# Optimization experiments

Measured on AMD Instinct MI355X. Metric: run time of the kernel, lower is better.

## Reference

```python
import jax, jax.numpy as jnp
import numpy as np

N, C, H, W = 8, 256, 52, 52
N_WIN, NUM_HEADS, TOPK = 7, 1, 4
RS = (H // N_WIN, W // N_WIN)  # region size (7, 7)
SCALE = C ** -0.5


def _avg_pool_ceil(t):
    # F.avg_pool2d(kernel=RS, stride=RS, ceil_mode=True, count_include_pad=False)
    B, Ch, h_in, w_in = t.shape
    h = -(-h_in // RS[0]); w = -(-w_in // RS[1])
    tp = jnp.pad(t, ((0, 0), (0, 0), (0, h * RS[0] - h_in), (0, w * RS[1] - w_in)))
    s = tp.reshape(B, Ch, h, RS[0], w, RS[1]).sum(axis=(3, 5))
    rc = np.minimum(RS[0], h_in - np.arange(h) * RS[0]).astype(np.float32)
    cc = np.minimum(RS[1], w_in - np.arange(w) * RS[1]).astype(np.float32)
    return s / (rc[:, None] * cc[None, :])


def _nearest_up(t):
    # F.interpolate(mode='nearest', scale_factor=RS) for integer scales == repeat
    return jnp.repeat(jnp.repeat(t, RS[0], axis=2), RS[1], axis=3)


def _grid2seq(t):
    # BCHW -> (B, nhead, nregion, reg_area, head_dim)
    B, Ch, Hp, Wp = t.shape
    rh, rw = Hp // RS[0], Wp // RS[1]
    hd = Ch // NUM_HEADS
    t = t.reshape(B, NUM_HEADS, hd, rh, RS[0], rw, RS[1]).transpose(0, 1, 3, 5, 4, 6, 2)
    return t.reshape(B, NUM_HEADS, rh * rw, RS[0] * RS[1], hd), rh, rw


def _forward(x, y, q_w, q_b, k_w, k_b):
    q = jnp.einsum('nchw,oc->nohw', x, q_w) + q_b[None, :, None, None]
    k = jnp.einsum('nchw,oc->nohw', y, k_w) + k_b[None, :, None, None]
    # routing path uses detached q, k
    q_r = _avg_pool_ceil(jax.lax.stop_gradient(q))  # (B, C, 8, 8)
    k_r = _avg_pool_ceil(jax.lax.stop_gradient(k))
    B, _, h, w = q_r.shape
    nreg = h * w
    a_r = jnp.einsum('nchw,ncyx->nhwyx', q_r, k_r).reshape(B, nreg, nreg)
    idx = jax.lax.top_k(a_r, TOPK)[1]                              # (B, nreg, topk)
    idx = jnp.broadcast_to(idx[:, None], (B, NUM_HEADS, nreg, TOPK))
    a_r = SCALE * a_r
    # coarse scores upsampled over key pixels, then over query pixels
    a1 = _nearest_up(a_r.reshape(B, nreg, h, w))                   # (B, nreg, Hp, Wp)
    Hp, Wp = a1.shape[2], a1.shape[3]
    a1 = _nearest_up(a1.transpose(0, 2, 3, 1).reshape(B, Hp * Wp, h, w))  # (B, Hp*Wp, Hp, Wp)
    reg_area = (Hp * Wp) // nreg
    a6 = a1.reshape(B, NUM_HEADS, nreg, reg_area // NUM_HEADS, nreg, reg_area)
    # fine attention on padded q, k
    pad_b = (RS[0] - H % RS[0]) % RS[0]
    pad_r = (RS[1] - W % RS[1]) % RS[1]
    qp = jnp.pad(q, ((0, 0), (0, 0), (0, pad_b), (0, pad_r)))
    kp = jnp.pad(k, ((0, 0), (0, 0), (0, pad_b), (0, pad_r)))
    q_seq, rh, rw = _grid2seq(qp)   # (B, nh, nreg, reg_area, hd)
    k_seq, _, _ = _grid2seq(kp)
    bI = jnp.arange(B)[:, None, None, None]
    mI = jnp.arange(NUM_HEADS)[None, :, None, None]
    key_g = k_seq[bI, mI, idx]      # gather top-k key regions: (B, nh, nreg, topk, reg_area, hd)
    attn = jnp.einsum('bmrqd,bmrtkd->bmrqtk', q_seq * SCALE, key_g)
    # torch.scatter along dim 4 with index repeated over the t' axis -> duplicate
    # writes to the same slot; serial torch scatter keeps the LAST write (t'=TOPK-1)
    vals = attn[:, :, :, :TOPK, TOPK - 1, :]  # (B, nh, nreg, topk, reg_area)
    rI = jnp.arange(nreg)[None, None, :, None]
    tI = jnp.arange(TOPK)[None, None, None, :]
    corr = a6.at[bI, mI, rI, tI, idx].set(vals)
    # _corr2grid: 10-dim view + 'bmhwpqyxcd->bmhpwqycxd'
    c10 = corr.reshape(B, NUM_HEADS, rh, rw, RS[0], RS[1], rh, rw, RS[0], RS[1])
    c10 = c10.transpose(0, 1, 2, 4, 3, 5, 6, 8, 7, 9)
    Hf, Wf = rh * RS[0], rw * RS[1]
    corr = c10.reshape(B, NUM_HEADS, Hf, Wf, Hf, Wf)
    corr = corr[:, :, :Hf - pad_b, :Wf - pad_r, :Hf - pad_b, :Wf - pad_r]
    return corr.transpose(0, 2, 3, 1, 4, 5)  # (B, H, W, nhead, H, W)


def setup_inputs():
    ks = jax.random.split(jax.random.key(0), 6)
    return {
        'x': jax.random.normal(ks[0], (N, C, H, W), jnp.float32),
        'y': jax.random.normal(ks[1], (N, C, H, W), jnp.float32),
        'q_w': jax.random.normal(ks[2], (C, C), jnp.float32) * (C ** -0.5),
        'q_b': jax.random.normal(ks[3], (C,), jnp.float32) * 0.02,
        'k_w': jax.random.normal(ks[4], (C, C), jnp.float32) * (C ** -0.5),
        'k_b': jax.random.normal(ks[5], (C,), jnp.float32) * 0.02,
    }


def reference(x, y, q_w, q_b, k_w, k_b):
    return _forward(x, y, q_w, q_b, k_w, k_b)
```

## Files before the change

kernel.cpp:

```cpp
#include <hip/hip_runtime.h>

#define NB 8
#define C 256
#define HW 52
#define P (HW*HW)
#define NREG 64
#define NTOPK 4
#define SCALE 0.0625f

static __device__ __forceinline__ int d7(int v)  { return (v*9363) >> 16; }
static __device__ __forceinline__ int d56(int v) { return (v*18725) >> 20; }
static __device__ __forceinline__ int d13(int v) { return (v*10083) >> 17; }

__global__ __launch_bounds__(256) void k1_pool_prep_tr(
    const float* __restrict__ x, const float* __restrict__ y,
    const float* __restrict__ qw, const float* __restrict__ qb,
    const float* __restrict__ kw, const float* __restrict__ kb,
    float* __restrict__ xr, float* __restrict__ yr, float* __restrict__ xg,
    float* __restrict__ M, float* __restrict__ u, float* __restrict__ v2,
    float* __restrict__ c0p, float* __restrict__ yT)
{
    __shared__ float sm[4*P];
    const int tid = threadIdx.x;
    const int bx = blockIdx.x;

    if (bx >= 1089) {
        const int tb = bx - 1089;
        const int b = tb / 172;
        const int rem = tb - b*172;
        const int ct = rem / 43;
        const int pt = rem - ct*43;
        const int c0 = ct*64, pos0 = pt*64;
        float* tile = sm;
        const float* ysrc = y + ((size_t)(b*256 + c0))*P;
        #pragma unroll
        for (int p = 0; p < 4; p++) {
            const int cr = p*16 + (tid>>4);
            const int f4 = tid&15;
            const int pos = pos0 + f4*4;
            if (pos < P) {
                const float4 v = *(const float4*)(ysrc + (size_t)cr*P + pos);
                float* d = tile + cr*65 + f4*4;
                d[0]=v.x; d[1]=v.y; d[2]=v.z; d[3]=v.w;
            }
        }
        __syncthreads();
        #pragma unroll
        for (int p = 0; p < 4; p++) {
            const int pj = p*16 + (tid>>4);
            const int c4 = tid&15;
            const int pos = pos0 + pj;
            if (pos < P) {
                float4 v;
                v.x = tile[(c4*4+0)*65 + pj];
                v.y = tile[(c4*4+1)*65 + pj];
                v.z = tile[(c4*4+2)*65 + pj];
                v.w = tile[(c4*4+3)*65 + pj];
                *(float4*)(yT + ((size_t)(b*P + pos))*256 + c0 + c4*4) = v;
            }
        }
        return;
    }

    if (bx >= 1024) {
        const int pb = bx - 1024;
        if (pb == 64) {
            float ua = 0.f, va = 0.f;
            for (int e = 0; e < 256; e++) {
                ua += qb[e] * kw[e*256 + tid];
                va += kb[e] * qw[e*256 + tid];
            }
            u[tid] = ua; v2[tid] = va;
            if (tid == 0) {
                float c = 0.f;
                for (int e = 0; e < 256; e++) c += qb[e]*kb[e];
                c0p[0] = c;
            }
            return;
        }
        const int cx0 = pb * 4;
        float (*wqs)[4] = (float(*)[4])sm;
        *(float4*)&wqs[tid][0] = *(const float4*)(qw + tid*256 + cx0);
        __syncthreads();
        float a0=0.f, a1=0.f, a2=0.f, a3=0.f;
        #pragma unroll 4
        for (int o = 0; o < 256; o++) {
            const float wk = kw[o*256 + tid];
            const float4 wq = *(const float4*)&wqs[o][0];
            a0 += wq.x*wk; a1 += wq.y*wk; a2 += wq.z*wk; a3 += wq.w*wk;
        }
        M[(cx0+0)*256 + tid] = a0;
        M[(cx0+1)*256 + tid] = a1;
        M[(cx0+2)*256 + tid] = a2;
        M[(cx0+3)*256 + tid] = a3;
        return;
    }

    const int w = tid >> 6, lane = tid & 63;
    const int pl = bx*4 + w;
    const int proj = pl >> 11;
    const int bcid = pl & 2047;
    const float* src = (proj ? y : x) + (size_t)bcid * P;
    float* plane = sm + w*P;
    {
        const float4* s4 = (const float4*)src;
        float4* p4 = (float4*)plane;
        for (int g = lane; g < 676; g += 64) p4[g] = s4[g];
    }
    __syncthreads();
    const int jh = lane >> 3, jw = lane & 7;
    const int y0 = jh*7, x0 = jw*7;
    const int ry = min(7, HW - y0), rx = min(7, HW - x0);
    float s = 0.f;
    for (int dy = 0; dy < ry; ++dy) {
        const float* row = plane + (y0 + dy)*HW + x0;
        for (int dx = 0; dx < rx; ++dx) s += row[dx];
    }
    (proj ? yr : xr)[bcid*64 + lane] = s / (float)(ry*rx);
    if (!proj) {
        const float* r0 = plane + y0*HW + x0;
        float4 g4;
        g4.x = r0[0]; g4.y = r0[1]; g4.z = r0[2];
        g4.w = (x0 + 3 < HW) ? r0[3] : 0.f;
        *(float4*)&xg[bcid*256 + lane*4] = g4;
    }
}

__global__ __launch_bounds__(256) void k2_gemms(
    const float* __restrict__ xr, const float* __restrict__ yr,
    const float* __restrict__ qw, const float* __restrict__ qb,
    const float* __restrict__ kw, const float* __restrict__ kb,
    float* __restrict__ qr, float* __restrict__ kr,
    const float* __restrict__ xg, const float* __restrict__ M,
    const float* __restrict__ u, float* __restrict__ G)
{
    __shared__ float As[32][64];
    __shared__ float Bs[32][64];
    const int tid = threadIdx.x;
    const int tx = tid & 15, ty = tid >> 4;

    float acc[4][4];
    #pragma unroll
    for (int i = 0; i < 4; i++)
        #pragma unroll
        for (int j = 0; j < 4; j++) acc[i][j] = 0.f;

    if (blockIdx.x < 64) {
        const int bp = blockIdx.x >> 2;
        const int b = bp >> 1, proj = bp & 1;
        const float* X = (proj ? yr : xr) + b*C*64;
        const float* W = proj ? kw : qw;
        const float* Bv = proj ? kb : qb;
        float* O = (proj ? kr : qr) + b*C*64;
        const int o0 = (blockIdx.x & 3) * 64;

        const int aor = tid & 63;
        const int akc = (tid >> 6) * 8;
        const int bkr = tid >> 3;
        const int bjc = (tid & 7) * 8;

        for (int k0 = 0; k0 < 256; k0 += 32) {
            const float4 w0 = *(const float4*)(W + (o0 + aor)*256 + k0 + akc);
            const float4 w1 = *(const float4*)(W + (o0 + aor)*256 + k0 + akc + 4);
            const float4 x0v = *(const float4*)(X + (k0 + bkr)*64 + bjc);
            const float4 x1v = *(const float4*)(X + (k0 + bkr)*64 + bjc + 4);
            __syncthreads();
            As[akc+0][aor] = w0.x; As[akc+1][aor] = w0.y; As[akc+2][aor] = w0.z; As[akc+3][aor] = w0.w;
            As[akc+4][aor] = w1.x; As[akc+5][aor] = w1.y; As[akc+6][aor] = w1.z; As[akc+7][aor] = w1.w;
            *(float4*)&Bs[bkr][bjc] = x0v;
            *(float4*)&Bs[bkr][bjc+4] = x1v;
            __syncthreads();
            #pragma unroll
            for (int kk = 0; kk < 32; kk++) {
                const float4 a = *(const float4*)&As[kk][ty*4];
                const float4 bb = *(const float4*)&Bs[kk][tx*4];
                const float av[4] = {a.x, a.y, a.z, a.w};
                const float bv[4] = {bb.x, bb.y, bb.z, bb.w};
                #pragma unroll
                for (int i = 0; i < 4; i++)
                    #pragma unroll
                    for (int j = 0; j < 4; j++) acc[i][j] += av[i]*bv[j];
            }
        }
        #pragma unroll
        for (int i = 0; i < 4; i++) {
            const int o = o0 + ty*4 + i;
            const float bias = Bv[o];
            float4 ov;
            ov.x = acc[i][0]+bias; ov.y = acc[i][1]+bias;
            ov.z = acc[i][2]+bias; ov.w = acc[i][3]+bias;
            *(float4*)(O + o*64 + tx*4) = ov;
        }
    } else {
        const int id2 = blockIdx.x - 64;
        const int b = id2 >> 4, sub = id2 & 15;
        const int p0 = (sub >> 2)*64, o0 = (sub & 3)*64;
        const float* Xg = xg + b*C*256;
        float* Gb = G + b*256*256;

        const int lkr = tid >> 3;
        const int ljc = (tid & 7) * 8;

        for (int k0 = 0; k0 < 256; k0 += 32) {
            const float4 a0 = *(const float4*)(Xg + (k0 + lkr)*256 + p0 + ljc);
            const float4 a1 = *(const float4*)(Xg + (k0 + lkr)*256 + p0 + ljc + 4);
            const float4 b0 = *(const float4*)(M + (k0 + lkr)*256 + o0 + ljc);
            const float4 b1 = *(const float4*)(M + (k0 + lkr)*256 + o0 + ljc + 4);
            __syncthreads();
            *(float4*)&As[lkr][ljc] = a0; *(float4*)&As[lkr][ljc+4] = a1;
            *(float4*)&Bs[lkr][ljc] = b0; *(float4*)&Bs[lkr][ljc+4] = b1;
            __syncthreads();
            #pragma unroll
            for (int kk = 0; kk < 32; kk++) {
                const float4 a = *(const float4*)&As[kk][ty*4];
                const float4 bb = *(const float4*)&Bs[kk][tx*4];
                const float av[4] = {a.x, a.y, a.z, a.w};
                const float bv[4] = {bb.x, bb.y, bb.z, bb.w};
                #pragma unroll
                for (int i = 0; i < 4; i++)
                    #pragma unroll
                    for (int j = 0; j < 4; j++) acc[i][j] += av[i]*bv[j];
            }
        }
        const float4 u4 = *(const float4*)(u + o0 + tx*4);
        #pragma unroll
        for (int i = 0; i < 4; i++) {
            float4 ov;
            ov.x = acc[i][0]+u4.x; ov.y = acc[i][1]+u4.y;
            ov.z = acc[i][2]+u4.z; ov.w = acc[i][3]+u4.w;
            *(float4*)(Gb + (p0 + ty*4 + i)*256 + o0 + tx*4) = ov;
        }
    }
}

__global__ __launch_bounds__(256) void k3_topk_vals(
    const float* __restrict__ yT, const float* __restrict__ qr,
    const float* __restrict__ kr, const float* __restrict__ G,
    const float* __restrict__ xg, const float* __restrict__ v2,
    const float* __restrict__ c0p,
    float* __restrict__ arT, int* __restrict__ idxout, float* __restrict__ vals)
{
    const int b = blockIdx.y, r = blockIdx.x;
    __shared__ float pdot[4][64];
    __shared__ float Gs[4][256];
    __shared__ float Hs[4];
    __shared__ int gsh;
    __shared__ float Ys[49][260];
    const int tid = threadIdx.x, w = tid >> 6, lane = tid & 63;

    {
        const float* qcol = qr + b*C*64 + r;
        const float* kcol = kr + b*C*64 + lane;
        float d = 0.f;
        #pragma unroll 8
        for (int cc = 0; cc < 64; cc++) {
            const int c = w*64 + cc;
            d += qcol[c*64] * kcol[c*64];
        }
        pdot[w][lane] = d;
    }
    *(float4*)&Gs[w][lane*4] = *(const float4*)(G + ((b*256 + r*4 + w)*256) + lane*4);
    {
        const int pos = r*4 + w;
        float acc = 0.f;
        #pragma unroll
        for (int cc = 0; cc < 4; cc++) {
            const int c = lane + cc*64;
            acc += xg[(b*256 + c)*256 + pos] * v2[c];
        }
        #pragma unroll
        for (int off = 32; off >= 1; off >>= 1) acc += __shfl_xor(acc, off);
        if (lane == 0) Hs[w] = acc + c0p[0];
    }
    __syncthreads();

    if (w == 0) {
        const float dot = pdot[0][lane] + pdot[1][lane] + pdot[2][lane] + pdot[3][lane];
        arT[(b*64 + lane)*64 + r] = dot * SCALE;
        float v = dot;
        const int my = lane;
        #pragma unroll
        for (int t = 0; t < NTOPK; t++) {
            float bv = v; int bi = my;
            #pragma unroll
            for (int off = 32; off >= 1; off >>= 1) {
                const float ov = __shfl_xor(bv, off);
                const int   oi = __shfl_xor(bi, off);
                if (ov > bv || (ov == bv && oi < bi)) { bv = ov; bi = oi; }
            }
            if (lane == 0) {
                idxout[(b*64 + r)*NTOPK + t] = bi;
                if (t == NTOPK-1) gsh = bi;
            }
            if (my == bi) v = -3.0e38f;
        }
    }
    __syncthreads();

    const int g = gsh;
    const int gy = g >> 3, gx = g & 7;
    for (int i = tid; i < 49*64; i += 256) {
        const int k2 = i >> 6, f4 = i & 63;
        const int dy = d7(k2), dx = k2 - dy*7;
        const int kY = gy*7 + dy, kX = gx*7 + dx;
        float4 v = make_float4(0.f, 0.f, 0.f, 0.f);
        if (kY < HW && kX < HW)
            v = *(const float4*)(yT + ((size_t)(b*P + kY*HW + kX))*256 + f4*4);
        *(float4*)&Ys[k2][f4*4] = v;
    }
    __syncthreads();

    if (tid < NTOPK*49) {
        const int t = tid / 49, k2 = tid % 49;
        const int qX = (r & 7)*7 + t;
        const int dy = d7(k2), dx = k2 - dy*7;
        const int kY = gy*7 + dy, kX = gx*7 + dx;
        float res = 0.f;
        if (qX < HW && kY < HW && kX < HW) {
            const float4* Gp = (const float4*)&Gs[t][0];
            const float4* Yp = (const float4*)&Ys[k2][0];
            float dot = 0.f;
            #pragma unroll 8
            for (int cc = 0; cc < 64; cc++) {
                const float4 a = Gp[cc], yy = Yp[cc];
                dot += a.x*yy.x + a.y*yy.y + a.z*yy.z + a.w*yy.w;
            }
            res = SCALE * (dot + Hs[t]);
        }
        vals[((b*64 + r)*NTOPK + t)*49 + k2] = res;
    }
}

__global__ __launch_bounds__(256) void fill_kernel(
    const float* __restrict__ arT, const float* __restrict__ vals,
    const int* __restrict__ idx, float* __restrict__ out)
{
    const int b = blockIdx.y;
    const int yx = blockIdx.x;
    const int Y1 = yx / HW, X1 = yx % HW;
    const int r1 = (Y1/7)*8 + X1/7;
    const int q1 = (Y1%7)*7 + X1%7;
    const int p2 = r1*49 + q1;
    const int yy = p2/56, xx = p2 - 56*yy;
    const int regB = (yy/7)*8 + xx/7;

    __shared__ float acol[64];
    __shared__ float vrow[49];
    const int tid = threadIdx.x;
    if (tid < 64) acol[tid] = arT[(b*64 + regB)*64 + tid];
    int ovr = -1;
    if (q1 < NTOPK) {
        ovr = idx[(b*64 + r1)*NTOPK + q1];
        if (tid < 49) vrow[tid] = vals[((b*64 + r1)*NTOPK + q1)*49 + tid];
    }
    __syncthreads();

    float* plane = out + (size_t)(b*P + yx) * P;
    for (int u = tid; u < 676; u += 256) {
        const int Y2 = d13(u);
        const int g4 = u - Y2*13;
        const int X2b = g4*4;
        const int ry2 = d7(Y2);
        const int my2 = Y2 - ry2*7;
        float res[4];
        #pragma unroll
        for (int j = 0; j < 4; j++) {
            const int X2 = X2b + j;
            const int rx2 = d7(X2);
            const int mx2 = X2 - rx2*7;
            const int r2 = ry2*8 + rx2;
            const int k2 = my2*7 + mx2;
            const int P1 = r2*49 + k2;
            const int Yp = d56(P1);
            const int Xp = P1 - Yp*56;
            const int regA = d7(Yp)*8 + d7(Xp);
            float v = acol[regA];
            if (r2 == ovr) v = vrow[k2];
            res[j] = v;
        }
        float4 o; o.x = res[0]; o.y = res[1]; o.z = res[2]; o.w = res[3];
        *(float4*)(plane + Y2*HW + X2b) = o;
    }
}

extern "C" void kernel_launch(void* const* d_in, const int* in_sizes, int n_in,
                              void* d_out, int out_size, void* d_ws, size_t ws_size,
                              hipStream_t stream)
{
    const float* x  = (const float*)d_in[0];
    const float* y  = (const float*)d_in[1];
    const float* qw = (const float*)d_in[2];
    const float* qb = (const float*)d_in[3];
    const float* kw = (const float*)d_in[4];
    const float* kb = (const float*)d_in[5];
    float* out = (float*)d_out;

    float* xr  = out;
    float* yr  = xr + 131072;
    float* qr  = yr + 131072;
    float* kr  = qr + 131072;
    float* xg  = kr + 131072;
    float* G   = xg + 524288;
    float* M   = G  + 524288;
    float* u   = M  + 65536;
    float* v2  = u  + 256;
    float* c0p = v2 + 256;
    float* yT  = c0p + 16;

    float* ws  = (float*)d_ws;
    float* arT = ws;
    float* vls = arT + 32768;
    int*   idx = (int*)(vls + 100352);

    k1_pool_prep_tr<<<2465, 256, 0, stream>>>(x, y, qw, qb, kw, kb, xr, yr, xg,
                                              M, u, v2, c0p, yT);
    k2_gemms<<<192, 256, 0, stream>>>(xr, yr, qw, qb, kw, kb, qr, kr, xg, M, u, G);
    k3_topk_vals<<<dim3(64, 8), 256, 0, stream>>>(yT, qr, kr, G, xg, v2, c0p, arT, idx, vls);
    fill_kernel<<<dim3(P, 8), 256, 0, stream>>>(arT, vls, idx, out);
}
```

Baseline: 112.6 us.

## Fuse all stages into one cooperative persistent kernel with algebraic routing GEMM

Replaces the four kernel launches with a single cooperative kernel of 512 persistent blocks that uses grid.sync between the prep, GEMM, top-k and fill phases. The routing score is now computed as xr·M plus bias terms, which removes the separate q/k projection GEMMs. The goal is to cut launch gaps and one GEMM stage. The cost is grid-wide barriers and a persistent fill loop with fewer resident blocks, which may reduce store throughput. A fallback to the old multi-kernel path is kept in case the cooperative launch fails.

```diff
diff --git a/kernel.cpp b/kernel.cpp
--- a/kernel.cpp
+++ b/kernel.cpp
@@ -1,16 +1,360 @@
 #include <hip/hip_runtime.h>
+#include <hip/hip_cooperative_groups.h>
+
+namespace cg = cooperative_groups;
 
 #define NB 8
 #define C 256
 #define HW 52
 #define P (HW*HW)
-#define NREG 64
 #define NTOPK 4
 #define SCALE 0.0625f
 
 static __device__ __forceinline__ int d7(int v)  { return (v*9363) >> 16; }
 static __device__ __forceinline__ int d56(int v) { return (v*18725) >> 20; }
 static __device__ __forceinline__ int d13(int v) { return (v*10083) >> 17; }
+
+#define OFF_XR 0
+#define OFF_YR 131072
+#define OFF_XG 262144
+#define OFF_G  786432
+#define OFF_GR 1310720
+#define OFF_M  1441792
+#define OFF_U  1507328
+#define OFF_V2 1507584
+#define OFF_C0 1507840
+#define OFF_YT 1507856
+
+__global__ __launch_bounds__(256, 2) void mega(
+    const float* __restrict__ x, const float* __restrict__ y,
+    const float* __restrict__ qw, const float* __restrict__ qb,
+    const float* __restrict__ kw, const float* __restrict__ kb,
+    float* __restrict__ out, float* __restrict__ ws)
+{
+    cg::grid_group grid = cg::this_grid();
+    __shared__ float sm[14032];
+    const int tid = threadIdx.x;
+    const int bid = blockIdx.x;
+    const int w = tid >> 6, lane = tid & 63;
+
+    float* xr = out + OFF_XR;
+    float* yr = out + OFF_YR;
+    float* xg = out + OFF_XG;
+    float* G  = out + OFF_G;
+    float* Gr = out + OFF_GR;
+    float* M  = out + OFF_M;
+    float* uu = out + OFF_U;
+    float* v2 = out + OFF_V2;
+    float* c0 = out + OFF_C0;
+    float* yT = out + OFF_YT;
+    float* arT = ws;
+    float* vls = ws + 32768;
+    int*   idx = (int*)(ws + 133120);
+
+    for (int un = bid; un < 2465; un += 512) {
+        __syncthreads();
+        if (un < 65) {
+            const int pb = un;
+            if (pb == 64) {
+                float ua = 0.f, va = 0.f;
+                for (int e = 0; e < 256; e++) {
+                    ua += qb[e] * kw[e*256 + tid];
+                    va += kb[e] * qw[e*256 + tid];
+                }
+                uu[tid] = ua; v2[tid] = va;
+                if (tid == 0) {
+                    float cc = 0.f;
+                    for (int e = 0; e < 256; e++) cc += qb[e]*kb[e];
+                    c0[0] = cc;
+                }
+            } else {
+                const int cx0 = pb * 4;
+                float (*wqs)[4] = (float(*)[4])sm;
+                *(float4*)&wqs[tid][0] = *(const float4*)(qw + tid*256 + cx0);
+                __syncthreads();
+                float a0=0.f, a1=0.f, a2=0.f, a3=0.f;
+                #pragma unroll 4
+                for (int o = 0; o < 256; o++) {
+                    const float wk = kw[o*256 + tid];
+                    const float4 wq = *(const float4*)&wqs[o][0];
+                    a0 += wq.x*wk; a1 += wq.y*wk; a2 += wq.z*wk; a3 += wq.w*wk;
+                }
+                M[(cx0+0)*256 + tid] = a0;
+                M[(cx0+1)*256 + tid] = a1;
+                M[(cx0+2)*256 + tid] = a2;
+                M[(cx0+3)*256 + tid] = a3;
+            }
+        } else if (un < 1089) {
+            const int pl = (un - 65)*4 + w;
+            const int proj = pl >> 11;
+            const int bcid = pl & 2047;
+            const float* src = (proj ? y : x) + (size_t)bcid * P;
+            float* plane = sm + w*P;
+            {
+                const float4* s4 = (const float4*)src;
+                float4* p4 = (float4*)plane;
+                for (int g = lane; g < 676; g += 64) p4[g] = s4[g];
+            }
+            __syncthreads();
+            const int jh = lane >> 3, jw = lane & 7;
+            const int y0 = jh*7, x0 = jw*7;
+            const int ry = min(7, HW - y0), rx = min(7, HW - x0);
+            float s = 0.f;
+            for (int dy = 0; dy < ry; ++dy) {
+                const float* row = plane + (y0 + dy)*HW + x0;
+                for (int dx = 0; dx < rx; ++dx) s += row[dx];
+            }
+            (proj ? yr : xr)[bcid*64 + lane] = s / (float)(ry*rx);
+            if (!proj) {
+                const float* r0 = plane + y0*HW + x0;
+                float4 g4;
+                g4.x = r0[0]; g4.y = r0[1]; g4.z = r0[2];
+                g4.w = (x0 + 3 < HW) ? r0[3] : 0.f;
+                *(float4*)&xg[bcid*256 + lane*4] = g4;
+            }
+        } else {
+            const int tb = un - 1089;
+            const int b = tb / 172;
+            const int rem = tb - b*172;
+            const int ct = rem / 43;
+            const int pt = rem - ct*43;
+            const int cc0 = ct*64, pos0 = pt*64;
+            float* tile = sm;
+            const float* ysrc = y + ((size_t)(b*256 + cc0))*P;
+            #pragma unroll
+            for (int p = 0; p < 4; p++) {
+                const int cr = p*16 + (tid>>4);
+                const int f4 = tid&15;
+                const int pos = pos0 + f4*4;
+                if (pos < P) {
+                    const float4 v = *(const float4*)(ysrc + (size_t)cr*P + pos);
+                    float* d = tile + cr*65 + f4*4;
+                    d[0]=v.x; d[1]=v.y; d[2]=v.z; d[3]=v.w;
+                }
+            }
+            __syncthreads();
+            #pragma unroll
+            for (int p = 0; p < 4; p++) {
+                const int pj = p*16 + (tid>>4);
+                const int c4 = tid&15;
+                const int pos = pos0 + pj;
+                if (pos < P) {
+                    float4 v;
+                    v.x = tile[(c4*4+0)*65 + pj];
+                    v.y = tile[(c4*4+1)*65 + pj];
+                    v.z = tile[(c4*4+2)*65 + pj];
+                    v.w = tile[(c4*4+3)*65 + pj];
+                    *(float4*)(yT + ((size_t)(b*P + pos))*256 + cc0 + c4*4) = v;
+                }
+            }
+        }
+    }
+    grid.sync();
+
+    for (int un = bid; un < 160; un += 512) {
+        const int b = un / 20;
+        const int rem = un - b*20;
+        const int pt = rem >> 2, ot = rem & 3;
+        const int o0 = ot*64;
+        float* As = sm;
+        float* Bs = sm + 2048;
+        const int tx = tid & 15, ty = tid >> 4;
+        float acc[4][4];
+        #pragma unroll
+        for (int i = 0; i < 4; i++)
+            #pragma unroll
+            for (int j = 0; j < 4; j++) acc[i][j] = 0.f;
+
+        const int lkr = tid >> 3;
+        const int ljc = (tid & 7) * 8;
+        const float* Asrc; int astr;
+        if (pt < 4) { Asrc = xg + (size_t)b*C*256 + pt*64; astr = 256; }
+        else        { Asrc = xr + (size_t)b*C*64;          astr = 64;  }
+
+        for (int k0 = 0; k0 < 256; k0 += 32) {
+            const float4 a0 = *(const float4*)(Asrc + (k0 + lkr)*astr + ljc);
+            const float4 a1 = *(const float4*)(Asrc + (k0 + lkr)*astr + ljc + 4);
+            const float4 b0 = *(const float4*)(M + (k0 + lkr)*256 + o0 + ljc);
+            const float4 b1 = *(const float4*)(M + (k0 + lkr)*256 + o0 + ljc + 4);
+            __syncthreads();
+            *(float4*)&As[lkr*64 + ljc] = a0; *(float4*)&As[lkr*64 + ljc + 4] = a1;
+            *(float4*)&Bs[lkr*64 + ljc] = b0; *(float4*)&Bs[lkr*64 + ljc + 4] = b1;
+            __syncthreads();
+            #pragma unroll
+            for (int kk = 0; kk < 32; kk++) {
+                const float4 a = *(const float4*)&As[kk*64 + ty*4];
+                const float4 bb = *(const float4*)&Bs[kk*64 + tx*4];
+                const float av[4] = {a.x, a.y, a.z, a.w};
+                const float bv[4] = {bb.x, bb.y, bb.z, bb.w};
+                #pragma unroll
+                for (int i = 0; i < 4; i++)
+                    #pragma unroll
+                    for (int j = 0; j < 4; j++) acc[i][j] += av[i]*bv[j];
+            }
+        }
+        const float4 u4 = *(const float4*)(uu + o0 + tx*4);
+        float* base = (pt < 4) ? (G + ((size_t)b*256 + pt*64)*256)
+                               : (Gr + (size_t)b*64*256);
+        #pragma unroll
+        for (int i = 0; i < 4; i++) {
+            float4 ov;
+            ov.x = acc[i][0]+u4.x; ov.y = acc[i][1]+u4.y;
+            ov.z = acc[i][2]+u4.z; ov.w = acc[i][3]+u4.w;
+            *(float4*)(base + (ty*4 + i)*256 + o0 + tx*4) = ov;
+        }
+        __syncthreads();
+    }
+    grid.sync();
+
+    {
+        const int b = bid >> 6, r = bid & 63;
+        float* Ys   = sm;
+        float* Gs   = sm + 12740;
+        float* pdot = sm + 13764;
+        float* aux  = sm + 14020;
+
+        {
+            const float* GrRow = Gr + ((size_t)b*64 + r)*256;
+            const float* yrB = yr + b*C*64;
+            const float* xrB = xr + b*C*64;
+            float d = 0.f, av = 0.f;
+            #pragma unroll 8
+            for (int cc = 0; cc < 64; cc++) {
+                const int c = w*64 + cc;
+                const float g = GrRow[c];
+                d += g * yrB[c*64 + lane];
+                av += v2[c] * xrB[c*64 + r];
+            }
+            pdot[w*64 + lane] = d;
+            if (lane == 0) aux[4 + w] = av;
+        }
+        *(float4*)&Gs[w*256 + lane*4] =
+            *(const float4*)(G + ((size_t)(b*256 + r*4 + w))*256 + lane*4);
+        {
+            const int pos = r*4 + w;
+            float acc = 0.f;
+            #pragma unroll
+            for (int cc = 0; cc < 4; cc++) {
+                const int c = lane + cc*64;
+                acc += xg[((size_t)(b*256 + c))*256 + pos] * v2[c];
+            }
+            #pragma unroll
+            for (int off = 32; off >= 1; off >>= 1) acc += __shfl_xor(acc, off);
+            if (lane == 0) aux[w] = acc + c0[0];
+        }
+        __syncthreads();
+
+        if (w == 0) {
+            const float ci = aux[4] + aux[5] + aux[6] + aux[7] + c0[0];
+            const float dot = pdot[lane] + pdot[64+lane] + pdot[128+lane]
+                            + pdot[192+lane] + ci;
+            arT[(b*64 + lane)*64 + r] = dot * SCALE;
+            float v = dot;
+            const int my = lane;
+            #pragma unroll
+            for (int t = 0; t < NTOPK; t++) {
+                float bv = v; int bi = my;
+                #pragma unroll
+                for (int off = 32; off >= 1; off >>= 1) {
+                    const float ov = __shfl_xor(bv, off);
+                    const int   oi = __shfl_xor(bi, off);
+                    if (ov > bv || (ov == bv && oi < bi)) { bv = ov; bi = oi; }
+                }
+                if (lane == 0) {
+                    idx[(b*64 + r)*NTOPK + t] = bi;
+                    if (t == NTOPK-1) ((int*)aux)[8] = bi;
+                }
+                if (my == bi) v = -3.0e38f;
+            }
+        }
+        __syncthreads();
+
+        const int g = ((int*)aux)[8];
+        const int gy = g >> 3, gx = g & 7;
+        for (int i = tid; i < 49*64; i += 256) {
+            const int k2 = i >> 6, f4 = i & 63;
+            const int dy = d7(k2), dx = k2 - dy*7;
+            const int kY = gy*7 + dy, kX = gx*7 + dx;
+            float4 v = make_float4(0.f, 0.f, 0.f, 0.f);
+            if (kY < HW && kX < HW)
+                v = *(const float4*)(yT + ((size_t)(b*P + kY*HW + kX))*256 + f4*4);
+            *(float4*)&Ys[k2*260 + f4*4] = v;
+        }
+        __syncthreads();
+
+        if (tid < NTOPK*49) {
+            const int t = tid / 49, k2 = tid - (tid/49)*49;
+            const int qX = (r & 7)*7 + t;
+            const int dy = d7(k2), dx = k2 - dy*7;
+            const int kY = gy*7 + dy, kX = gx*7 + dx;
+            float res = 0.f;
+            if (qX < HW && kY < HW && kX < HW) {
+                const float4* Gp = (const float4*)&Gs[t*256];
+                const float4* Yp = (const float4*)&Ys[k2*260];
+                float dot = 0.f;
+                #pragma unroll 8
+                for (int cc = 0; cc < 64; cc++) {
+                    const float4 a = Gp[cc], yy = Yp[cc];
+                    dot += a.x*yy.x + a.y*yy.y + a.z*yy.z + a.w*yy.w;
+                }
+                res = SCALE * (dot + aux[t]);
+            }
+            vls[((b*64 + r)*NTOPK + t)*49 + k2] = res;
+        }
+    }
+    grid.sync();
+
+    {
+        float* acol = sm;
+        float* vrow = sm + 64;
+        for (int un = bid; un < NB*P; un += 512) {
+            __syncthreads();
+            const int b = un / P;
+            const int yx = un - b*P;
+            const int Y1 = yx / HW, X1 = yx - (yx/HW)*HW;
+            const int r1 = (Y1/7)*8 + X1/7;
+            const int q1 = (Y1%7)*7 + X1%7;
+            const int p2 = r1*49 + q1;
+            const int yy = p2/56, xx = p2 - 56*yy;
+            const int regB = (yy/7)*8 + xx/7;
+
+            if (tid < 64) acol[tid] = arT[(b*64 + regB)*64 + tid];
+            int ovr = -1;
+            if (q1 < NTOPK) {
+                ovr = idx[(b*64 + r1)*NTOPK + q1];
+                if (tid < 49) vrow[tid] = vls[((b*64 + r1)*NTOPK + q1)*49 + tid];
+            }
+            __syncthreads();
+
+            float* plane = out + (size_t)(b*P + yx) * P;
+            for (int u = tid; u < 676; u += 256) {
+                const int Y2 = d13(u);
+                const int g4 = u - Y2*13;
+                const int X2b = g4*4;
+                const int ry2 = d7(Y2);
+                const int my2 = Y2 - ry2*7;
+                float res[4];
+                #pragma unroll
+                for (int j = 0; j < 4; j++) {
+                    const int X2 = X2b + j;
+                    const int rx2 = d7(X2);
+                    const int mx2 = X2 - rx2*7;
+                    const int r2 = ry2*8 + rx2;
+                    const int k2 = my2*7 + mx2;
+                    const int P1 = r2*49 + k2;
+                    const int Yp = d56(P1);
+                    const int Xp = P1 - Yp*56;
+                    const int regA = d7(Yp)*8 + d7(Xp);
+                    float v = acol[regA];
+                    if (r2 == ovr) v = vrow[k2];
+                    res[j] = v;
+                }
+                float4 o; o.x = res[0]; o.y = res[1]; o.z = res[2]; o.w = res[3];
+                *(float4*)(plane + Y2*HW + X2b) = o;
+            }
+        }
+    }
+}
 
 __global__ __launch_bounds__(256) void k1_pool_prep_tr(
     const float* __restrict__ x, const float* __restrict__ y,
@@ -61,7 +405,6 @@
         }
         return;
     }
-
     if (bx >= 1024) {
         const int pb = bx - 1024;
         if (pb == 64) {
@@ -95,7 +438,6 @@
         M[(cx0+3)*256 + tid] = a3;
         return;
     }
-
     const int w = tid >> 6, lane = tid & 63;
     const int pl = bx*4 + w;
     const int proj = pl >> 11;
@@ -138,7 +480,6 @@
     __shared__ float Bs[32][64];
     const int tid = threadIdx.x;
     const int tx = tid & 15, ty = tid >> 4;
-
     float acc[4][4];
     #pragma unroll
     for (int i = 0; i < 4; i++)
@@ -153,12 +494,10 @@
         const float* Bv = proj ? kb : qb;
         float* O = (proj ? kr : qr) + b*C*64;
         const int o0 = (blockIdx.x & 3) * 64;
-
         const int aor = tid & 63;
         const int akc = (tid >> 6) * 8;
         const int bkr = tid >> 3;
         const int bjc = (tid & 7) * 8;
-
         for (int k0 = 0; k0 < 256; k0 += 32) {
             const float4 w0 = *(const float4*)(W + (o0 + aor)*256 + k0 + akc);
             const float4 w1 = *(const float4*)(W + (o0 + aor)*256 + k0 + akc + 4);
@@ -197,10 +536,8 @@
         const int p0 = (sub >> 2)*64, o0 = (sub & 3)*64;
         const float* Xg = xg + b*C*256;
         float* Gb = G + b*256*256;
-
         const int lkr = tid >> 3;
         const int ljc = (tid & 7) * 8;
-
         for (int k0 = 0; k0 < 256; k0 += 32) {
             const float4 a0 = *(const float4*)(Xg + (k0 + lkr)*256 + p0 + ljc);
             const float4 a1 = *(const float4*)(Xg + (k0 + lkr)*256 + p0 + ljc + 4);
@@ -247,7 +584,6 @@
     __shared__ int gsh;
     __shared__ float Ys[49][260];
     const int tid = threadIdx.x, w = tid >> 6, lane = tid & 63;
-
     {
         const float* qcol = qr + b*C*64 + r;
         const float* kcol = kr + b*C*64 + lane;
@@ -273,7 +609,6 @@
         if (lane == 0) Hs[w] = acc + c0p[0];
     }
     __syncthreads();
-
     if (w == 0) {
         const float dot = pdot[0][lane] + pdot[1][lane] + pdot[2][lane] + pdot[3][lane];
         arT[(b*64 + lane)*64 + r] = dot * SCALE;
@@ -296,7 +631,6 @@
         }
     }
     __syncthreads();
-
     const int g = gsh;
     const int gy = g >> 3, gx = g & 7;
     for (int i = tid; i < 49*64; i += 256) {
@@ -309,7 +643,6 @@
         *(float4*)&Ys[k2][f4*4] = v;
     }
     __syncthreads();
-
     if (tid < NTOPK*49) {
         const int t = tid / 49, k2 = tid % 49;
         const int qX = (r & 7)*7 + t;
@@ -343,7 +676,6 @@
     const int p2 = r1*49 + q1;
     const int yy = p2/56, xx = p2 - 56*yy;
     const int regB = (yy/7)*8 + xx/7;
-
     __shared__ float acol[64];
     __shared__ float vrow[49];
     const int tid = threadIdx.x;
@@ -354,7 +686,6 @@
         if (tid < 49) vrow[tid] = vals[((b*64 + r1)*NTOPK + q1)*49 + tid];
     }
     __syncthreads();
-
     float* plane = out + (size_t)(b*P + yx) * P;
     for (int u = tid; u < 676; u += 256) {
         const int Y2 = d13(u);
@@ -394,27 +725,39 @@
     const float* kw = (const float*)d_in[4];
     const float* kb = (const float*)d_in[5];
     float* out = (float*)d_out;
-
-    float* xr  = out;
-    float* yr  = xr + 131072;
-    float* qr  = yr + 131072;
-    float* kr  = qr + 131072;
-    float* xg  = kr + 131072;
-    float* G   = xg + 524288;
-    float* M   = G  + 524288;
-    float* u   = M  + 65536;
-    float* v2  = u  + 256;
-    float* c0p = v2 + 256;
-    float* yT  = c0p + 16;
-
     float* ws  = (float*)d_ws;
-    float* arT = ws;
-    float* vls = arT + 32768;
-    int*   idx = (int*)(vls + 100352);
-
-    k1_pool_prep_tr<<<2465, 256, 0, stream>>>(x, y, qw, qb, kw, kb, xr, yr, xg,
-                                              M, u, v2, c0p, yT);
-    k2_gemms<<<192, 256, 0, stream>>>(xr, yr, qw, qb, kw, kb, qr, kr, xg, M, u, G);
-    k3_topk_vals<<<dim3(64, 8), 256, 0, stream>>>(yT, qr, kr, G, xg, v2, c0p, arT, idx, vls);
-    fill_kernel<<<dim3(P, 8), 256, 0, stream>>>(arT, vls, idx, out);
+
+    const float* xp = x; const float* yp = y;
+    const float* qwp = qw; const float* qbp = qb;
+    const float* kwp = kw; const float* kbp = kb;
+    float* outp = out; float* wsp = ws;
+    void* args[8] = { (void*)&xp, (void*)&yp, (void*)&qwp, (void*)&qbp,
+                      (void*)&kwp, (void*)&kbp, (void*)&outp, (void*)&wsp };
+
+    hipError_t err = hipLaunchCooperativeKernel(
+        reinterpret_cast<const void*>(&mega), dim3(512), dim3(256),
+        args, 0u, stream);
+
+    if (err != hipSuccess) {
+        float* xr  = out;
+        float* yr  = xr + 131072;
+        float* qr  = yr + 131072;
+        float* kr  = qr + 131072;
+        float* xg  = kr + 131072;
+        float* G   = xg + 524288;
+        float* M   = G  + 524288;
+        float* u   = M  + 65536;
+        float* v2  = u  + 256;
+        float* c0p = v2 + 256;
+        float* yT  = c0p + 16;
+        float* arT = ws;
+        float* vls = arT + 32768;
+        int*   idx = (int*)(vls + 100352);
+
+        k1_pool_prep_tr<<<2465, 256, 0, stream>>>(x, y, qw, qb, kw, kb, xr, yr, xg,
+                                                  M, u, v2, c0p, yT);
+        k2_gemms<<<192, 256, 0, stream>>>(xr, yr, qw, qb, kw, kb, qr, kr, xg, M, u, G);
+        k3_topk_vals<<<dim3(64, 8), 256, 0, stream>>>(yT, qr, kr, G, xg, v2, c0p, arT, idx, vls);
+        fill_kernel<<<dim3(P, 8), 256, 0, stream>>>(arT, vls, idx, out);
+    }
 }
```

Result: slower. 321.1 us (+185.2%).

## Fold GEMM kernel into top-k kernel by routing through bilinear matrix M

Applied to the files above, without the earlier changes.

Removes the separate GEMM launch. Each top-k block now computes its own G rows, plus the pooled-query row, by multiplying transposed pooled/gathered x against the precomputed M = Wq^T Wk matrix. The routing score is recomputed as x_r^T M y_r plus bias terms, so the separate q and k projections are no longer needed. The cost is redundant per-block matvec work and strided transposed writes in the pooling kernel, in exchange for one fewer launch and fewer intermediate round trips through memory.

```diff
diff --git a/kernel.cpp b/kernel.cpp
--- a/kernel.cpp
+++ b/kernel.cpp
@@ -4,25 +4,40 @@
 #define C 256
 #define HW 52
 #define P (HW*HW)
-#define NREG 64
 #define NTOPK 4
 #define SCALE 0.0625f
 
 static __device__ __forceinline__ int d7(int v)  { return (v*9363) >> 16; }
 static __device__ __forceinline__ int d56(int v) { return (v*18725) >> 20; }
 static __device__ __forceinline__ int d13(int v) { return (v*10083) >> 17; }
+
+#define OFF_YR  0
+#define OFF_XGT 131072
+#define OFF_XRT 655360
+#define OFF_M   786432
+#define OFF_U   851968
+#define OFF_V2  852224
+#define OFF_C0  852480
+#define OFF_YT  852496
 
 __global__ __launch_bounds__(256) void k1_pool_prep_tr(
     const float* __restrict__ x, const float* __restrict__ y,
     const float* __restrict__ qw, const float* __restrict__ qb,
     const float* __restrict__ kw, const float* __restrict__ kb,
-    float* __restrict__ xr, float* __restrict__ yr, float* __restrict__ xg,
-    float* __restrict__ M, float* __restrict__ u, float* __restrict__ v2,
-    float* __restrict__ c0p, float* __restrict__ yT)
+    float* __restrict__ scr)
 {
     __shared__ float sm[4*P];
     const int tid = threadIdx.x;
     const int bx = blockIdx.x;
+
+    float* yr  = scr + OFF_YR;
+    float* xgT = scr + OFF_XGT;
+    float* xrT = scr + OFF_XRT;
+    float* M   = scr + OFF_M;
+    float* u   = scr + OFF_U;
+    float* v2  = scr + OFF_V2;
+    float* c0p = scr + OFF_C0;
+    float* yT  = scr + OFF_YT;
 
     if (bx >= 1089) {
         const int tb = bx - 1089;
@@ -100,6 +115,7 @@
     const int pl = bx*4 + w;
     const int proj = pl >> 11;
     const int bcid = pl & 2047;
+    const int bb = bcid >> 8, cc = bcid & 255;
     const float* src = (proj ? y : x) + (size_t)bcid * P;
     float* plane = sm + w*P;
     {
@@ -116,166 +132,98 @@
         const float* row = plane + (y0 + dy)*HW + x0;
         for (int dx = 0; dx < rx; ++dx) s += row[dx];
     }
-    (proj ? yr : xr)[bcid*64 + lane] = s / (float)(ry*rx);
-    if (!proj) {
+    const float pooled = s / (float)(ry*rx);
+    if (proj) {
+        yr[bcid*64 + lane] = pooled;
+    } else {
+        xrT[((size_t)(bb*64) + lane)*256 + cc] = pooled;
         const float* r0 = plane + y0*HW + x0;
-        float4 g4;
-        g4.x = r0[0]; g4.y = r0[1]; g4.z = r0[2];
-        g4.w = (x0 + 3 < HW) ? r0[3] : 0.f;
-        *(float4*)&xg[bcid*256 + lane*4] = g4;
+        #pragma unroll
+        for (int t = 0; t < 4; t++) {
+            const float v = (x0 + t < HW) ? r0[t] : 0.f;
+            xgT[((size_t)(bb*256) + lane*4 + t)*256 + cc] = v;
+        }
     }
 }
 
-__global__ __launch_bounds__(256) void k2_gemms(
-    const float* __restrict__ xr, const float* __restrict__ yr,
-    const float* __restrict__ qw, const float* __restrict__ qb,
-    const float* __restrict__ kw, const float* __restrict__ kb,
-    float* __restrict__ qr, float* __restrict__ kr,
-    const float* __restrict__ xg, const float* __restrict__ M,
-    const float* __restrict__ u, float* __restrict__ G)
-{
-    __shared__ float As[32][64];
-    __shared__ float Bs[32][64];
-    const int tid = threadIdx.x;
-    const int tx = tid & 15, ty = tid >> 4;
-
-    float acc[4][4];
-    #pragma unroll
-    for (int i = 0; i < 4; i++)
-        #pragma unroll
-        for (int j = 0; j < 4; j++) acc[i][j] = 0.f;
-
-    if (blockIdx.x < 64) {
-        const int bp = blockIdx.x >> 2;
-        const int b = bp >> 1, proj = bp & 1;
-        const float* X = (proj ? yr : xr) + b*C*64;
-        const float* W = proj ? kw : qw;
-        const float* Bv = proj ? kb : qb;
-        float* O = (proj ? kr : qr) + b*C*64;
-        const int o0 = (blockIdx.x & 3) * 64;
-
-        const int aor = tid & 63;
-        const int akc = (tid >> 6) * 8;
-        const int bkr = tid >> 3;
-        const int bjc = (tid & 7) * 8;
-
-        for (int k0 = 0; k0 < 256; k0 += 32) {
-            const float4 w0 = *(const float4*)(W + (o0 + aor)*256 + k0 + akc);
-            const float4 w1 = *(const float4*)(W + (o0 + aor)*256 + k0 + akc + 4);
-            const float4 x0v = *(const float4*)(X + (k0 + bkr)*64 + bjc);
-            const float4 x1v = *(const float4*)(X + (k0 + bkr)*64 + bjc + 4);
-            __syncthreads();
-            As[akc+0][aor] = w0.x; As[akc+1][aor] = w0.y; As[akc+2][aor] = w0.z; As[akc+3][aor] = w0.w;
-            As[akc+4][aor] = w1.x; As[akc+5][aor] = w1.y; As[akc+6][aor] = w1.z; As[akc+7][aor] = w1.w;
-            *(float4*)&Bs[bkr][bjc] = x0v;
-            *(float4*)&Bs[bkr][bjc+4] = x1v;
-            __syncthreads();
-            #pragma unroll
-            for (int kk = 0; kk < 32; kk++) {
-                const float4 a = *(const float4*)&As[kk][ty*4];
-                const float4 bb = *(const float4*)&Bs[kk][tx*4];
-                const float av[4] = {a.x, a.y, a.z, a.w};
-                const float bv[4] = {bb.x, bb.y, bb.z, bb.w};
-                #pragma unroll
-                for (int i = 0; i < 4; i++)
-                    #pragma unroll
-                    for (int j = 0; j < 4; j++) acc[i][j] += av[i]*bv[j];
-            }
-        }
-        #pragma unroll
-        for (int i = 0; i < 4; i++) {
-            const int o = o0 + ty*4 + i;
-            const float bias = Bv[o];
-            float4 ov;
-            ov.x = acc[i][0]+bias; ov.y = acc[i][1]+bias;
-            ov.z = acc[i][2]+bias; ov.w = acc[i][3]+bias;
-            *(float4*)(O + o*64 + tx*4) = ov;
-        }
-    } else {
-        const int id2 = blockIdx.x - 64;
-        const int b = id2 >> 4, sub = id2 & 15;
-        const int p0 = (sub >> 2)*64, o0 = (sub & 3)*64;
-        const float* Xg = xg + b*C*256;
-        float* Gb = G + b*256*256;
-
-        const int lkr = tid >> 3;
-        const int ljc = (tid & 7) * 8;
-
-        for (int k0 = 0; k0 < 256; k0 += 32) {
-            const float4 a0 = *(const float4*)(Xg + (k0 + lkr)*256 + p0 + ljc);
-            const float4 a1 = *(const float4*)(Xg + (k0 + lkr)*256 + p0 + ljc + 4);
-            const float4 b0 = *(const float4*)(M + (k0 + lkr)*256 + o0 + ljc);
-            const float4 b1 = *(const float4*)(M + (k0 + lkr)*256 + o0 + ljc + 4);
-            __syncthreads();
-            *(float4*)&As[lkr][ljc] = a0; *(float4*)&As[lkr][ljc+4] = a1;
-            *(float4*)&Bs[lkr][ljc] = b0; *(float4*)&Bs[lkr][ljc+4] = b1;
-            __syncthreads();
-            #pragma unroll
-            for (int kk = 0; kk < 32; kk++) {
-                const float4 a = *(const float4*)&As[kk][ty*4];
-                const float4 bb = *(const float4*)&Bs[kk][tx*4];
-                const float av[4] = {a.x, a.y, a.z, a.w};
-                const float bv[4] = {bb.x, bb.y, bb.z, bb.w};
-                #pragma unroll
-                for (int i = 0; i < 4; i++)
-                    #pragma unroll
-                    for (int j = 0; j < 4; j++) acc[i][j] += av[i]*bv[j];
-            }
-        }
-        const float4 u4 = *(const float4*)(u + o0 + tx*4);
-        #pragma unroll
-        for (int i = 0; i < 4; i++) {
-            float4 ov;
-            ov.x = acc[i][0]+u4.x; ov.y = acc[i][1]+u4.y;
-            ov.z = acc[i][2]+u4.z; ov.w = acc[i][3]+u4.w;
-            *(float4*)(Gb + (p0 + ty*4 + i)*256 + o0 + tx*4) = ov;
-        }
-    }
-}
-
-__global__ __launch_bounds__(256) void k3_topk_vals(
-    const float* __restrict__ yT, const float* __restrict__ qr,
-    const float* __restrict__ kr, const float* __restrict__ G,
-    const float* __restrict__ xg, const float* __restrict__ v2,
-    const float* __restrict__ c0p,
+__global__ __launch_bounds__(256) void k2_topk_vals(
+    const float* __restrict__ scr,
     float* __restrict__ arT, int* __restrict__ idxout, float* __restrict__ vals)
 {
     const int b = blockIdx.y, r = blockIdx.x;
+    const int tid = threadIdx.x, w = tid >> 6, lane = tid & 63;
+
+    const float* yr  = scr + OFF_YR;
+    const float* xgT = scr + OFF_XGT;
+    const float* xrT = scr + OFF_XRT;
+    const float* M   = scr + OFF_M;
+    const float* u   = scr + OFF_U;
+    const float* v2  = scr + OFF_V2;
+    const float* c0p = scr + OFF_C0;
+    const float* yT  = scr + OFF_YT;
+
+    __shared__ float Gs[4][256];
+    __shared__ float Grs[256];
     __shared__ float pdot[4][64];
-    __shared__ float Gs[4][256];
-    __shared__ float Hs[4];
+    __shared__ float aux[12];
     __shared__ int gsh;
     __shared__ float Ys[49][260];
-    const int tid = threadIdx.x, w = tid >> 6, lane = tid & 63;
-
+
+    const float* xrow0 = xgT + ((size_t)(b*256) + r*4)*256;
+    const float* xrow4 = xrT + ((size_t)(b*64) + r)*256;
     {
-        const float* qcol = qr + b*C*64 + r;
-        const float* kcol = kr + b*C*64 + lane;
+        float a0=0.f, a1=0.f, a2=0.f, a3=0.f, a4=0.f;
+        #pragma unroll 4
+        for (int c = 0; c < 256; c++) {
+            const float m = M[c*256 + tid];
+            a0 += xrow0[c]       * m;
+            a1 += xrow0[256 + c] * m;
+            a2 += xrow0[512 + c] * m;
+            a3 += xrow0[768 + c] * m;
+            a4 += xrow4[c]       * m;
+        }
+        const float uo = u[tid];
+        Gs[0][tid] = a0 + uo;
+        Gs[1][tid] = a1 + uo;
+        Gs[2][tid] = a2 + uo;
+        Gs[3][tid] = a3 + uo;
+        Grs[tid]   = a4 + uo;
+    }
+    {
+        const float* xh = xrow0 + w*256;
+        float hacc = 0.f;
+        #pragma unroll
+        for (int j = 0; j < 4; j++) {
+            const int c = lane + j*64;
+            hacc += xh[c] * v2[c];
+        }
+        #pragma unroll
+        for (int off = 32; off >= 1; off >>= 1) hacc += __shfl_xor(hacc, off);
+        if (lane == 0) aux[w] = hacc + c0p[0];
+
+        float cacc = xrow4[w*64 + lane] * v2[w*64 + lane];
+        #pragma unroll
+        for (int off = 32; off >= 1; off >>= 1) cacc += __shfl_xor(cacc, off);
+        if (lane == 0) aux[4 + w] = cacc;
+    }
+    __syncthreads();
+
+    {
+        const float* yrB = yr + b*C*64;
         float d = 0.f;
         #pragma unroll 8
         for (int cc = 0; cc < 64; cc++) {
             const int c = w*64 + cc;
-            d += qcol[c*64] * kcol[c*64];
+            d += Grs[c] * yrB[c*64 + lane];
         }
         pdot[w][lane] = d;
     }
-    *(float4*)&Gs[w][lane*4] = *(const float4*)(G + ((b*256 + r*4 + w)*256) + lane*4);
-    {
-        const int pos = r*4 + w;
-        float acc = 0.f;
-        #pragma unroll
-        for (int cc = 0; cc < 4; cc++) {
-            const int c = lane + cc*64;
-            acc += xg[(b*256 + c)*256 + pos] * v2[c];
-        }
-        #pragma unroll
-        for (int off = 32; off >= 1; off >>= 1) acc += __shfl_xor(acc, off);
-        if (lane == 0) Hs[w] = acc + c0p[0];
-    }
     __syncthreads();
 
     if (w == 0) {
-        const float dot = pdot[0][lane] + pdot[1][lane] + pdot[2][lane] + pdot[3][lane];
+        const float ci = aux[4] + aux[5] + aux[6] + aux[7] + c0p[0];
+        const float dot = pdot[0][lane] + pdot[1][lane] + pdot[2][lane]
+                        + pdot[3][lane] + ci;
         arT[(b*64 + lane)*64 + r] = dot * SCALE;
         float v = dot;
         const int my = lane;
@@ -311,7 +259,7 @@
     __syncthreads();
 
     if (tid < NTOPK*49) {
-        const int t = tid / 49, k2 = tid % 49;
+        const int t = tid / 49, k2 = tid - (tid/49)*49;
         const int qX = (r & 7)*7 + t;
         const int dy = d7(k2), dx = k2 - dy*7;
         const int kY = gy*7 + dy, kX = gx*7 + dx;
@@ -325,7 +273,7 @@
                 const float4 a = Gp[cc], yy = Yp[cc];
                 dot += a.x*yy.x + a.y*yy.y + a.z*yy.z + a.w*yy.w;
             }
-            res = SCALE * (dot + Hs[t]);
+            res = SCALE * (dot + aux[t]);
         }
         vals[((b*64 + r)*NTOPK + t)*49 + k2] = res;
     }
@@ -395,26 +343,14 @@
     const float* kb = (const float*)d_in[5];
     float* out = (float*)d_out;
 
-    float* xr  = out;
-    float* yr  = xr + 131072;
-    float* qr  = yr + 131072;
-    float* kr  = qr + 131072;
-    float* xg  = kr + 131072;
-    float* G   = xg + 524288;
-    float* M   = G  + 524288;
-    float* u   = M  + 65536;
-    float* v2  = u  + 256;
-    float* c0p = v2 + 256;
-    float* yT  = c0p + 16;
+    float* scr = out;
 
     float* ws  = (float*)d_ws;
     float* arT = ws;
     float* vls = arT + 32768;
     int*   idx = (int*)(vls + 100352);
 
-    k1_pool_prep_tr<<<2465, 256, 0, stream>>>(x, y, qw, qb, kw, kb, xr, yr, xg,
-                                              M, u, v2, c0p, yT);
-    k2_gemms<<<192, 256, 0, stream>>>(xr, yr, qw, qb, kw, kb, qr, kr, xg, M, u, G);
-    k3_topk_vals<<<dim3(64, 8), 256, 0, stream>>>(yT, qr, kr, G, xg, v2, c0p, arT, idx, vls);
+    k1_pool_prep_tr<<<2465, 256, 0, stream>>>(x, y, qw, qb, kw, kb, scr);
+    k2_topk_vals<<<dim3(64, 8), 256, 0, stream>>>(scr, arT, idx, vls);
     fill_kernel<<<dim3(P, 8), 256, 0, stream>>>(arT, vls, idx, out);
 }
```

Measured after the change: 116.7 us. +3.7%, slower.
